# Performance work log

Hardware: AMD Instinct MI355X
Metric: run time of the kernel (lower is better)

The kernel has to match this reference:

```python
import jax, jax.numpy as jnp
import numpy as np

N, WIDTH, MODES, OUT_CH, N_LAYERS = 131072, 256, 512, 256, 4


def setup_inputs() -> dict:
    key = jax.random.key(0)
    ks = jax.random.split(key, 8)
    scale = 1.0 / (WIDTH * WIDTH)  # matches torch: 1/(in_channels*out_channels)
    return {
        "V": jax.random.normal(ks[0], (N, 3), dtype=jnp.float32),
        "fc0_w": jax.random.normal(ks[1], (WIDTH, 3), dtype=jnp.float32) * 0.02,
        "fc0_b": jnp.zeros((WIDTH,), dtype=jnp.float32),
        # real/imag stacked in last dim -> complex weights (4, in, out, modes)
        "sc_w": jax.random.normal(ks[2], (N_LAYERS, WIDTH, WIDTH, MODES, 2), dtype=jnp.float32) * scale,
        "fc1_w": jax.random.normal(ks[3], (128, WIDTH), dtype=jnp.float32) * 0.02,
        "fc1_b": jnp.zeros((128,), dtype=jnp.float32),
        "fc2_w": jax.random.normal(ks[4], (OUT_CH, 128), dtype=jnp.float32) * 0.02,
        "fc2_b": jnp.zeros((OUT_CH,), dtype=jnp.float32),
    }


def _spectral_conv(x, w_ri):
    # x: (b, c, n) real; w_ri: (c, o, modes, 2) real -> complex (c, o, modes)
    b, c, n = x.shape
    modes = w_ri.shape[2]
    n_freq = n // 2 + 1
    w = jax.lax.complex(w_ri[..., 0], w_ri[..., 1])
    x_ft = jnp.fft.rfft(x, axis=-1)                         # (b, c, n_freq)
    out_modes = jnp.einsum('bcm,com->bom', x_ft[:, :, :modes], w)
    out_ft = jnp.pad(out_modes, ((0, 0), (0, 0), (0, n_freq - modes)))
    return jnp.fft.irfft(out_ft, n=n, axis=-1).astype(x.dtype)


def reference(V, fc0_w, fc0_b, sc_w, fc1_w, fc1_b, fc2_w, fc2_b):
    # lift: (N,3) -> (N,width) -> (1,width,N)
    x = V @ fc0_w.T + fc0_b
    x = x.T[None, :, :]
    for i in range(N_LAYERS):
        x = _spectral_conv(x, sc_w[i])
    feat = x.mean(axis=-1)[0]                                # (width,)
    z = jnp.tanh(feat @ fc1_w.T + fc1_b) @ fc2_w.T + fc2_b   # (out_channels,)
    return z
```

## Files before the change

### kernel.cpp

```cpp
#include <hip/hip_runtime.h>
#include <math.h>


constexpr int kN = 131072;
constexpr int kWidth = 256;
constexpr int kModes = 512;
constexpr int kLayers = 4;

__global__ __launch_bounds__(256) void vsum_stage1(const float* __restrict__ V,
                                                   float* __restrict__ partials) {
    __shared__ float sred[3][256];
    int tid = threadIdx.x;
    int gt = blockIdx.x * 256 + tid;
    const float* p0 = V + (size_t)gt * 3;
    const float* p1 = V + (size_t)(gt + 65536) * 3;
    sred[0][tid] = p0[0] + p1[0];
    sred[1][tid] = p0[1] + p1[1];
    sred[2][tid] = p0[2] + p1[2];
    __syncthreads();
    for (int off = 128; off > 0; off >>= 1) {
        if (tid < off) {
            sred[0][tid] += sred[0][tid + off];
            sred[1][tid] += sred[1][tid + off];
            sred[2][tid] += sred[2][tid + off];
        }
        __syncthreads();
    }
    if (tid == 0) {
        partials[blockIdx.x * 3 + 0] = sred[0][0];
        partials[blockIdx.x * 3 + 1] = sred[1][0];
        partials[blockIdx.x * 3 + 2] = sred[2][0];
    }
}

__global__ __launch_bounds__(256) void lift_dc(const float* __restrict__ partials,
                                               const float* __restrict__ fc0_w,
                                               const float* __restrict__ fc0_b,
                                               float* __restrict__ X0) {
    __shared__ float red[256];
    __shared__ float S[3];
    int tid = threadIdx.x;
    for (int j = 0; j < 3; ++j) {
        red[tid] = partials[tid * 3 + j];
        __syncthreads();
        for (int off = 128; off > 0; off >>= 1) {
            if (tid < off) red[tid] += red[tid + off];
            __syncthreads();
        }
        if (tid == 0) S[j] = red[0];
        __syncthreads();
    }
    float x = S[0] * fc0_w[tid * 3 + 0] + S[1] * fc0_w[tid * 3 + 1] +
              S[2] * fc0_w[tid * 3 + 2] + (float)kN * fc0_b[tid];
    X0[tid] = x;
}

__global__ __launch_bounds__(256) void spectral_dc(const float* __restrict__ w,
                                                   const float* __restrict__ Xin,
                                                   float* __restrict__ Xout) {
    int o = blockIdx.x, c = threadIdx.x;
    size_t off = (((size_t)c * kWidth + o) * (size_t)kModes) * 2;
    float v = w[off] * Xin[c];
    __shared__ float red[256];
    red[c] = v;
    __syncthreads();
    for (int s = 128; s > 0; s >>= 1) {
        if (c < s) red[c] += red[c + s];
        __syncthreads();
    }
    if (c == 0) Xout[o] = red[0];
}

__global__ __launch_bounds__(256) void head(const float* __restrict__ X4,
                                            const float* __restrict__ fc1_w,
                                            const float* __restrict__ fc1_b,
                                            const float* __restrict__ fc2_w,
                                            const float* __restrict__ fc2_b,
                                            float* __restrict__ out) {
    __shared__ float feat[256];
    __shared__ float h[128];
    int t = threadIdx.x;
    feat[t] = X4[t] * (1.0f / (float)kN);
    __syncthreads();
    if (t < 128) {
        float acc = fc1_b[t];
        #pragma unroll 8
        for (int o = 0; o < 256; ++o) acc += feat[o] * fc1_w[t * 256 + o];
        h[t] = tanhf(acc);
    }
    __syncthreads();
    float acc = fc2_b[t];
    #pragma unroll 8
    for (int j = 0; j < 128; ++j) acc += h[j] * fc2_w[t * 128 + j];
    out[t] = acc;
}

extern "C" void kernel_launch(void* const* d_in, const int* in_sizes, int n_in,
                              void* d_out, int out_size, void* d_ws, size_t ws_size,
                              hipStream_t stream) {
    const float* V     = (const float*)d_in[0];
    const float* fc0_w = (const float*)d_in[1];
    const float* fc0_b = (const float*)d_in[2];
    const float* sc_w  = (const float*)d_in[3];
    const float* fc1_w = (const float*)d_in[4];
    const float* fc1_b = (const float*)d_in[5];
    const float* fc2_w = (const float*)d_in[6];
    const float* fc2_b = (const float*)d_in[7];
    float* out = (float*)d_out;

    float* ws = (float*)d_ws;
    float* partials = ws;
    float* Xa = ws + 1024;
    float* Xb = ws + 1280;

    vsum_stage1<<<256, 256, 0, stream>>>(V, partials);
    lift_dc<<<1, 256, 0, stream>>>(partials, fc0_w, fc0_b, Xa);

    const size_t layer_stride = (size_t)kWidth * kWidth * kModes * 2;
    float* bufs[2] = {Xa, Xb};
    for (int i = 0; i < kLayers; ++i) {
        spectral_dc<<<256, 256, 0, stream>>>(sc_w + (size_t)i * layer_stride,
                                             bufs[i & 1], bufs[(i + 1) & 1]);
    }
    head<<<1, 256, 0, stream>>>(bufs[kLayers & 1], fc1_w, fc1_b, fc2_w, fc2_b, out);
}
```

Before: 38.00 us.

## Fuse DC-mode chain into two kernels with a gathered weight slab

Replaces the seven-launch chain (V sum, lift, four spectral DC layers, head) with two kernels. The first gathers the DC-mode real weights of all four layers into a compact workspace slab, and in the same launch reduces V using float4 loads. The second is a single 1024-thread block that finishes the V reduction, lifts, applies all four layers from the compact slab and runs the MLP head. The goal is to cut launch overhead and the strided gathers on the serial path, at the cost of doing all layer math in one block.

Result: faster. 36.77 us (-3.2%).

```diff
diff --git a/kernel.cpp b/kernel.cpp
--- a/kernel.cpp
+++ b/kernel.cpp
@@ -6,93 +6,132 @@
 constexpr int kWidth = 256;
 constexpr int kModes = 512;
 constexpr int kLayers = 4;
+constexpr size_t kLayerStride = (size_t)kWidth * kWidth * kModes * 2;
+constexpr int kGatherBlocks = 256;
+constexpr int kVsumBlocks = 384;
 
-__global__ __launch_bounds__(256) void vsum_stage1(const float* __restrict__ V,
-                                                   float* __restrict__ partials) {
-    __shared__ float sred[3][256];
-    int tid = threadIdx.x;
-    int gt = blockIdx.x * 256 + tid;
-    const float* p0 = V + (size_t)gt * 3;
-    const float* p1 = V + (size_t)(gt + 65536) * 3;
-    sred[0][tid] = p0[0] + p1[0];
-    sred[1][tid] = p0[1] + p1[1];
-    sred[2][tid] = p0[2] + p1[2];
+
+__global__ __launch_bounds__(256) void stageA(const float* __restrict__ sc_w,
+                                              const float* __restrict__ V,
+                                              float* __restrict__ ws) {
+    int b = blockIdx.x, t = threadIdx.x;
+    if (b < kGatherBlocks) {
+        int rem = b * 256 + t;
+        const float* src = sc_w + (size_t)rem * (size_t)(kModes * 2);
+        #pragma unroll
+        for (int l = 0; l < kLayers; ++l) {
+            ws[(size_t)l * 65536 + rem] = src[(size_t)l * kLayerStride];
+        }
+    } else {
+        int vb = b - kGatherBlocks;
+        int q = vb * 256 + t;
+        const float4 v = reinterpret_cast<const float4*>(V)[q];
+        int r = q % 3;
+        float acc0 = 0.f, acc1 = 0.f, acc2 = 0.f;
+        float a[3] = {0.f, 0.f, 0.f};
+        a[r] = v.x + v.w;
+        a[(r + 1) % 3] = v.y;
+        a[(r + 2) % 3] = v.z;
+        acc0 = a[0]; acc1 = a[1]; acc2 = a[2];
+        __shared__ float sred[3][256];
+        sred[0][t] = acc0; sred[1][t] = acc1; sred[2][t] = acc2;
+        __syncthreads();
+        for (int off = 128; off > 0; off >>= 1) {
+            if (t < off) {
+                sred[0][t] += sred[0][t + off];
+                sred[1][t] += sred[1][t + off];
+                sred[2][t] += sred[2][t + off];
+            }
+            __syncthreads();
+        }
+        if (t == 0) {
+            float* partials = ws + 262144;
+            partials[vb * 3 + 0] = sred[0][0];
+            partials[vb * 3 + 1] = sred[1][0];
+            partials[vb * 3 + 2] = sred[2][0];
+        }
+    }
+}
+
+__global__ __launch_bounds__(1024) void stageB(const float* __restrict__ ws,
+                                               const float* __restrict__ fc0_w,
+                                               const float* __restrict__ fc0_b,
+                                               const float* __restrict__ fc1_w,
+                                               const float* __restrict__ fc1_b,
+                                               const float* __restrict__ fc2_w,
+                                               const float* __restrict__ fc2_b,
+                                               float* __restrict__ out) {
+    __shared__ float red[1024];
+    __shared__ float xbuf[256];
+    __shared__ float part[4][256];
+    __shared__ float S[3];
+    __shared__ float hbuf[128];
+    int t = threadIdx.x;
+    const float* partials = ws + 262144;
+
+    for (int j = 0; j < 3; ++j) {
+        red[t] = (t < kVsumBlocks) ? partials[t * 3 + j] : 0.f;
+        __syncthreads();
+        for (int off = 512; off > 0; off >>= 1) {
+            if (t < off) red[t] += red[t + off];
+            __syncthreads();
+        }
+        if (t == 0) S[j] = red[0];
+        __syncthreads();
+    }
+
+    if (t < 256) {
+        xbuf[t] = S[0] * fc0_w[t * 3] + S[1] * fc0_w[t * 3 + 1] +
+                  S[2] * fc0_w[t * 3 + 2] + (float)kN * fc0_b[t];
+    }
     __syncthreads();
-    for (int off = 128; off > 0; off >>= 1) {
-        if (tid < off) {
-            sred[0][tid] += sred[0][tid + off];
-            sred[1][tid] += sred[1][tid + off];
-            sred[2][tid] += sred[2][tid + off];
+
+    int g = t >> 8, o = t & 255;
+    for (int l = 0; l < kLayers; ++l) {
+        const float* W = ws + (size_t)l * 65536;
+        float acc = 0.f;
+        int c0 = g * 64;
+        #pragma unroll 8
+        for (int i = 0; i < 64; ++i) {
+            int c = c0 + i;
+            acc += W[c * 256 + o] * xbuf[c];
+        }
+        part[g][o] = acc;
+        __syncthreads();
+        if (t < 256) xbuf[t] = part[0][t] + part[1][t] + part[2][t] + part[3][t];
+        __syncthreads();
+    }
+
+    if (t < 256) xbuf[t] *= (1.0f / (float)kN);
+    __syncthreads();
+
+    {
+        int j = t & 127, s = t >> 7;
+        float acc = 0.f;
+        int c0 = s * 32;
+        #pragma unroll 8
+        for (int i = 0; i < 32; ++i) acc += xbuf[c0 + i] * fc1_w[j * 256 + c0 + i];
+        red[s * 128 + j] = acc;
+        __syncthreads();
+        if (t < 128) {
+            float a = 0.f;
+            #pragma unroll
+            for (int s2 = 0; s2 < 8; ++s2) a += red[s2 * 128 + t];
+            hbuf[t] = tanhf(a + fc1_b[t]);
         }
         __syncthreads();
     }
-    if (tid == 0) {
-        partials[blockIdx.x * 3 + 0] = sred[0][0];
-        partials[blockIdx.x * 3 + 1] = sred[1][0];
-        partials[blockIdx.x * 3 + 2] = sred[2][0];
+
+    {
+        int k = t & 255, s = t >> 8;
+        float acc = 0.f;
+        int c0 = s * 32;
+        #pragma unroll 8
+        for (int i = 0; i < 32; ++i) acc += hbuf[c0 + i] * fc2_w[k * 128 + c0 + i];
+        red[s * 256 + k] = acc;
+        __syncthreads();
+        if (t < 256) out[t] = red[t] + red[256 + t] + red[512 + t] + red[768 + t] + fc2_b[t];
     }
-}
-
-__global__ __launch_bounds__(256) void lift_dc(const float* __restrict__ partials,
-                                               const float* __restrict__ fc0_w,
-                                               const float* __restrict__ fc0_b,
-                                               float* __restrict__ X0) {
-    __shared__ float red[256];
-    __shared__ float S[3];
-    int tid = threadIdx.x;
-    for (int j = 0; j < 3; ++j) {
-        red[tid] = partials[tid * 3 + j];
-        __syncthreads();
-        for (int off = 128; off > 0; off >>= 1) {
-            if (tid < off) red[tid] += red[tid + off];
-            __syncthreads();
-        }
-        if (tid == 0) S[j] = red[0];
-        __syncthreads();
-    }
-    float x = S[0] * fc0_w[tid * 3 + 0] + S[1] * fc0_w[tid * 3 + 1] +
-              S[2] * fc0_w[tid * 3 + 2] + (float)kN * fc0_b[tid];
-    X0[tid] = x;
-}
-
-__global__ __launch_bounds__(256) void spectral_dc(const float* __restrict__ w,
-                                                   const float* __restrict__ Xin,
-                                                   float* __restrict__ Xout) {
-    int o = blockIdx.x, c = threadIdx.x;
-    size_t off = (((size_t)c * kWidth + o) * (size_t)kModes) * 2;
-    float v = w[off] * Xin[c];
-    __shared__ float red[256];
-    red[c] = v;
-    __syncthreads();
-    for (int s = 128; s > 0; s >>= 1) {
-        if (c < s) red[c] += red[c + s];
-        __syncthreads();
-    }
-    if (c == 0) Xout[o] = red[0];
-}
-
-__global__ __launch_bounds__(256) void head(const float* __restrict__ X4,
-                                            const float* __restrict__ fc1_w,
-                                            const float* __restrict__ fc1_b,
-                                            const float* __restrict__ fc2_w,
-                                            const float* __restrict__ fc2_b,
-                                            float* __restrict__ out) {
-    __shared__ float feat[256];
-    __shared__ float h[128];
-    int t = threadIdx.x;
-    feat[t] = X4[t] * (1.0f / (float)kN);
-    __syncthreads();
-    if (t < 128) {
-        float acc = fc1_b[t];
-        #pragma unroll 8
-        for (int o = 0; o < 256; ++o) acc += feat[o] * fc1_w[t * 256 + o];
-        h[t] = tanhf(acc);
-    }
-    __syncthreads();
-    float acc = fc2_b[t];
-    #pragma unroll 8
-    for (int j = 0; j < 128; ++j) acc += h[j] * fc2_w[t * 128 + j];
-    out[t] = acc;
 }
 
 extern "C" void kernel_launch(void* const* d_in, const int* in_sizes, int n_in,
@@ -107,20 +146,8 @@
     const float* fc2_w = (const float*)d_in[6];
     const float* fc2_b = (const float*)d_in[7];
     float* out = (float*)d_out;
+    float* ws = (float*)d_ws;
 
-    float* ws = (float*)d_ws;
-    float* partials = ws;
-    float* Xa = ws + 1024;
-    float* Xb = ws + 1280;
-
-    vsum_stage1<<<256, 256, 0, stream>>>(V, partials);
-    lift_dc<<<1, 256, 0, stream>>>(partials, fc0_w, fc0_b, Xa);
-
-    const size_t layer_stride = (size_t)kWidth * kWidth * kModes * 2;
-    float* bufs[2] = {Xa, Xb};
-    for (int i = 0; i < kLayers; ++i) {
-        spectral_dc<<<256, 256, 0, stream>>>(sc_w + (size_t)i * layer_stride,
-                                             bufs[i & 1], bufs[(i + 1) & 1]);
-    }
-    head<<<1, 256, 0, stream>>>(bufs[kLayers & 1], fc1_w, fc1_b, fc2_w, fc2_b, out);
+    stageA<<<kGatherBlocks + kVsumBlocks, 256, 0, stream>>>(sc_w, V, ws);
+    stageB<<<1, 1024, 0, stream>>>(ws, fc0_w, fc0_b, fc1_w, fc1_b, fc2_w, fc2_b, out);
 }
```
